# Performance work log

Hardware: AMD Instinct MI355X
Metric: run time of the kernel (lower is better)

The kernel has to match this reference:

```python
import jax, jax.numpy as jnp
import numpy as np

N = 20000          # num nodes
E = 320000         # num edges (avg degree 16)
IN = 128           # input feature dim
HID = 64           # layer1 out_channels per head
OUT = 128          # layer2 out_channels per head
H = 3              # attention heads
NEG = 0.15         # LeakyReLU negative slope
IN2 = IN + H * HID # layer2 input: concat(x, h1)


def setup_inputs() -> dict:
    key = jax.random.key(0)
    ks = jax.random.split(key, 12)
    lin = lambda k, fi, fo: (jax.random.normal(k, (fi, fo), jnp.float32) / np.float32(np.sqrt(fi)))
    return {
        "node_features": jax.random.normal(ks[0], (N, IN), jnp.float32),
        "Wl1": lin(ks[1], IN, H * HID),
        "bl1": jnp.zeros((H * HID,), jnp.float32),
        "Wr1": lin(ks[2], IN, H * HID),
        "br1": jnp.zeros((H * HID,), jnp.float32),
        "att1": jax.random.normal(ks[3], (H, HID), jnp.float32) / np.float32(np.sqrt(HID)),
        "bias1": jnp.zeros((H * HID,), jnp.float32),
        "Wl2": lin(ks[4], IN2, H * OUT),
        "bl2": jnp.zeros((H * OUT,), jnp.float32),
        "Wr2": lin(ks[5], IN2, H * OUT),
        "br2": jnp.zeros((H * OUT,), jnp.float32),
        "att2": jax.random.normal(ks[6], (H, OUT), jnp.float32) / np.float32(np.sqrt(OUT)),
        "bias2": jnp.zeros((OUT,), jnp.float32),
        "edge_index": jax.random.randint(ks[7], (2, E), 0, N, jnp.int64),
    }


def _gatv2(x, src, dst, Wl, bl, Wr, br, att, bias, concat):
    """PyG GATv2Conv (add_self_loops=False, eval/no dropout).
    src=edge_index[0] (message source j), dst=edge_index[1] (target i)."""
    n = x.shape[0]
    h, c = att.shape
    xl = (x @ Wl + bl).reshape(n, h, c)   # lin_l -> source/message features
    xr = (x @ Wr + br).reshape(n, h, c)   # lin_r -> target features
    e = xl[src] + xr[dst]                 # [E,H,C]
    e = jnp.where(e > 0, e, NEG * e)      # LeakyReLU
    logits = jnp.einsum('ehc,hc->eh', e, att)  # [E,H]
    # segment softmax over incoming edges of each dst node
    m = jax.ops.segment_max(logits, dst, num_segments=n)
    ex = jnp.exp(logits - m[dst])
    denom = jax.ops.segment_sum(ex, dst, num_segments=n)
    alpha = ex / (denom[dst] + 1e-16)
    out = jax.ops.segment_sum(xl[src] * alpha[:, :, None], dst, num_segments=n)  # [N,H,C]
    if concat:
        return out.reshape(n, h * c) + bias
    return out.mean(axis=1) + bias


def reference(node_features, Wl1, bl1, Wr1, br1, att1, bias1,
              Wl2, bl2, Wr2, br2, att2, bias2, edge_index):
    src, dst = edge_index[0], edge_index[1]
    h1 = jax.nn.relu(_gatv2(node_features, src, dst, Wl1, bl1, Wr1, br1, att1, bias1, True))
    h = jnp.concatenate([node_features, h1], axis=-1)  # [N, IN2]
    h2 = jax.nn.relu(_gatv2(h, src, dst, Wl2, bl2, Wr2, br2, att2, bias2, False))
    return h2
```

## Files before the change

kernel.cpp:

```cpp
#include <hip/hip_runtime.h>
#include <hip/hip_bf16.h>

#define NN 20000
#define EE 320000
#define IN 128
#define HID 64
#define OUTC 128
#define NH 3
#define NEG 0.15f
#define IN2 320
#define HO1 192
#define HO2 384
#define NB_SCAN 79
#define GRIDM128 157
#define LDA 72

typedef __hip_bfloat16 bf16;
typedef __attribute__((ext_vector_type(8))) short short8;
typedef __attribute__((ext_vector_type(4))) float f32x4;

__device__ __forceinline__ float bf2f(bf16 v) { return __bfloat162float(v); }
__device__ __forceinline__ bf16 f2bf(float v) { return __float2bfloat16(v); }
__device__ __forceinline__ float lrelu(float s) { return fmaxf(s, NEG * s); }
__device__ __forceinline__ float lo16(unsigned int d) {
    union { unsigned int u; float f; } c; c.u = d << 16; return c.f;
}
__device__ __forceinline__ float hi16(unsigned int d) {
    union { unsigned int u; float f; } c; c.u = d & 0xffff0000u; return c.f;
}

__global__ void k_count(const int* __restrict__ ei, int* __restrict__ cnt) {
    const int e = blockIdx.x * 256 + threadIdx.x;
    if (e < EE) atomicAdd(&cnt[ei[EE + e]], 1);
}

__global__ void k_scanA(const int* __restrict__ cnt, int* __restrict__ loc,
                        int* __restrict__ bsum) {
    __shared__ int sh[256];
    const int t = threadIdx.x;
    const int i = blockIdx.x * 256 + t;
    const int v = (i < NN) ? cnt[i] : 0;
    sh[t] = v; __syncthreads();
    for (int off = 1; off < 256; off <<= 1) {
        const int add = (t >= off) ? sh[t - off] : 0;
        __syncthreads();
        sh[t] += add; __syncthreads();
    }
    if (i < NN) loc[i] = sh[t];
    if (t == 255) bsum[blockIdx.x] = sh[255];
}

__global__ void k_scanB(int* __restrict__ bsum) {
    __shared__ int sh[128];
    const int t = threadIdx.x;
    const int v = (t < NB_SCAN) ? bsum[t] : 0;
    sh[t] = v; __syncthreads();
    for (int off = 1; off < 128; off <<= 1) {
        const int add = (t >= off) ? sh[t - off] : 0;
        __syncthreads();
        sh[t] += add; __syncthreads();
    }
    if (t < NB_SCAN) bsum[t] = sh[t] - v;
}

__global__ void k_scanC(const int* __restrict__ loc, const int* __restrict__ cnt,
                        const int* __restrict__ bsum, int* __restrict__ row_off,
                        int* __restrict__ fill) {
    const int i = blockIdx.x * 256 + threadIdx.x;
    if (i < NN) {
        const int ro = loc[i] - cnt[i] + bsum[blockIdx.x];
        row_off[i] = ro; fill[i] = ro;
    }
    if (i == 0) row_off[NN] = EE;
}

__global__ void k_scatter(const int* __restrict__ ei, int* __restrict__ fill,
                          int* __restrict__ csr_src) {
    const int e = blockIdx.x * 256 + threadIdx.x;
    if (e < EE) {
        const int p = atomicAdd(&fill[ei[EE + e]], 1);
        csr_src[p] = ei[e];
    }
}

__global__ void k_a2x(const float* __restrict__ x, bf16* __restrict__ xb) {
    const int idx = blockIdx.x * 256 + threadIdx.x;
    if (idx < NN * IN) xb[idx] = f2bf(x[idx]);
}

__global__ void k_wt(const float* __restrict__ Wl, const float* __restrict__ Wr,
                     int K, int NO, bf16* __restrict__ Wt) {
    const int idx = blockIdx.x * 256 + threadIdx.x;
    if (idx >= 2 * NO * K) return;
    const int n = idx / K, k = idx - n * K;
    const float* W = (n < NO) ? Wl : Wr;
    const int nn = (n < NO) ? n : n - NO;
    Wt[idx] = f2bf(W[(size_t)k * NO + nn]);
}

template <int K, int CH>
__launch_bounds__(256)
__global__ void gemm_mfma(const bf16* __restrict__ A0, int As0,
                          const bf16* __restrict__ A1, int As1,
                          const bf16* __restrict__ Wt,
                          const float* __restrict__ bl, const float* __restrict__ br,
                          int NO, size_t planeN,
                          bf16* __restrict__ outl, bf16* __restrict__ outr) {
    __shared__ bf16 Asm[128 * LDA];
    __shared__ bf16 Bsm[128 * LDA];
    const int tid = threadIdx.x;
    const int w = tid >> 6, lane = tid & 63;
    const int quad = lane >> 4, l15 = lane & 15;
    const int r0 = (w >> 1) * 64;
    const int c0 = (w & 1) * 64;
    const int m0 = blockIdx.x * 128;
    const int n0 = blockIdx.y * 128;

    f32x4 acc[4][4];
#pragma unroll
    for (int nt = 0; nt < 4; ++nt) {
        const int col = n0 + c0 + nt * 16 + l15;
        const float b = (col < NO) ? bl[col] : br[col - NO];
#pragma unroll
        for (int mt = 0; mt < 4; ++mt) acc[mt][nt] = (f32x4){b, b, b, b};
    }

    int arow[4]; size_t boff[4]; int soff[4];
#pragma unroll
    for (int q = 0; q < 4; ++q) {
        const int s = q * 256 + tid;
        int r = m0 + (s >> 3); if (r >= NN) r = NN - 1;
        arow[q] = r;
        boff[q] = (size_t)(n0 + (s >> 3)) * K + (s & 7) * 8;
        soff[q] = (s >> 3) * LDA + (s & 7) * 8;
    }

    short8 pa[4], pb[4];
#pragma unroll
    for (int q = 0; q < 4; ++q) {
        const int s = q * 256 + tid;
        pa[q] = *(const short8*)(A0 + (size_t)arow[q] * As0 + (s & 7) * 8);
        pb[q] = *(const short8*)(Wt + boff[q]);
    }

#pragma unroll
    for (int ks = 0; ks < K; ks += 64) {
#pragma unroll
        for (int q = 0; q < 4; ++q) {
            *(short8*)&Asm[soff[q]] = pa[q];
            *(short8*)&Bsm[soff[q]] = pb[q];
        }
        __syncthreads();
        if (ks + 64 < K) {
            const int nks = ks + 64;
#pragma unroll
            for (int q = 0; q < 4; ++q) {
                const int s = q * 256 + tid;
                const bf16* ap = (K <= 128 || nks < 128)
                    ? (A0 + (size_t)arow[q] * As0 + nks + (s & 7) * 8)
                    : (A1 + (size_t)arow[q] * As1 + (nks - 128) + (s & 7) * 8);
                pa[q] = *(const short8*)ap;
                pb[q] = *(const short8*)(Wt + boff[q] + nks);
            }
        }
#pragma unroll
        for (int kq = 0; kq < 2; ++kq) {
            short8 af[4], bf[4];
#pragma unroll
            for (int mt = 0; mt < 4; ++mt)
                af[mt] = *(const short8*)&Asm[(r0 + mt * 16 + l15) * LDA + kq * 32 + quad * 8];
#pragma unroll
            for (int nt = 0; nt < 4; ++nt)
                bf[nt] = *(const short8*)&Bsm[(c0 + nt * 16 + l15) * LDA + kq * 32 + quad * 8];
#pragma unroll
            for (int mt = 0; mt < 4; ++mt)
#pragma unroll
                for (int nt = 0; nt < 4; ++nt)
                    acc[mt][nt] = __builtin_amdgcn_mfma_f32_16x16x32_bf16(af[mt], bf[nt], acc[mt][nt], 0, 0, 0);
        }
        __syncthreads();
    }

#pragma unroll
    for (int mt = 0; mt < 4; ++mt)
#pragma unroll
    for (int nt = 0; nt < 4; ++nt) {
        const int col = n0 + c0 + nt * 16 + l15;
        const int cc = (col < NO) ? col : col - NO;
        bf16* o = (col < NO) ? outl : outr;
        const int h = cc / CH, c = cc - h * CH;
#pragma unroll
        for (int r = 0; r < 4; ++r) {
            const int row = m0 + r0 + mt * 16 + quad * 4 + r;
            if (row < NN) o[h * planeN + (size_t)row * CH + c] = f2bf(acc[mt][nt][r]);
        }
    }
}

__global__ void gather1(const int* __restrict__ row_off, const int* __restrict__ csr_src,
                        const bf16* __restrict__ xl, const bf16* __restrict__ xr,
                        const float* __restrict__ att, const float* __restrict__ bias,
                        bf16* __restrict__ h1) {
    const int i = blockIdx.x;
    const int w = threadIdx.x >> 6;
    const int lane = threadIdx.x & 63;
    const int g = lane >> 3;
    const int t = lane & 7;
    const unsigned short* xlu = (const unsigned short*)xl + (size_t)w * NN * HID;
    const unsigned short* xru = (const unsigned short*)xr + (size_t)w * NN * HID;
    float rv[8], av[8];
    {
        const uint4 ru = *(const uint4*)(xru + (size_t)i * HID + 8 * t);
        rv[0] = lo16(ru.x); rv[1] = hi16(ru.x);
        rv[2] = lo16(ru.y); rv[3] = hi16(ru.y);
        rv[4] = lo16(ru.z); rv[5] = hi16(ru.z);
        rv[6] = lo16(ru.w); rv[7] = hi16(ru.w);
#pragma unroll
        for (int c = 0; c < 8; ++c) av[c] = att[w * HID + 8 * t + c];
    }
    float acc[8] = {0.f, 0.f, 0.f, 0.f, 0.f, 0.f, 0.f, 0.f};
    float den = 0.f;
    const int kb = row_off[i], ke = row_off[i + 1];
    for (int p0 = kb; p0 < ke; p0 += 8) {
        const int idx = p0 + g;
        const int j = csr_src[idx < ke ? idx : ke - 1];
        const uint4 lu = *(const uint4*)(xlu + (size_t)j * HID + 8 * t);
        float lv[8];
        lv[0] = lo16(lu.x); lv[1] = hi16(lu.x);
        lv[2] = lo16(lu.y); lv[3] = hi16(lu.y);
        lv[4] = lo16(lu.z); lv[5] = hi16(lu.z);
        lv[6] = lo16(lu.w); lv[7] = hi16(lu.w);
        float p = 0.f;
#pragma unroll
        for (int c = 0; c < 8; ++c)
            p = fmaf(lrelu(lv[c] + rv[c]), av[c], p);
        p += __shfl_xor(p, 1, 64);
        p += __shfl_xor(p, 2, 64);
        p += __shfl_xor(p, 4, 64);
        const float ex = (idx < ke) ? __expf(p) : 0.f;
#pragma unroll
        for (int c = 0; c < 8; ++c) acc[c] = fmaf(ex, lv[c], acc[c]);
        den += ex;
    }
    __shared__ float part[NH][8][HID];
    __shared__ float dsh[NH][8];
    *(f32x4*)&part[w][g][8 * t]     = (f32x4){acc[0], acc[1], acc[2], acc[3]};
    *(f32x4*)&part[w][g][8 * t + 4] = (f32x4){acc[4], acc[5], acc[6], acc[7]};
    if (t == 0) dsh[w][g] = den;
    __syncthreads();
    const int o = threadIdx.x;
    const int hh = o >> 6, c = o & 63;
    float num = 0.f, dd = 0.f;
#pragma unroll
    for (int q = 0; q < 8; ++q) { num += part[hh][q][c]; dd += dsh[hh][q]; }
    const float v = num / (dd + 1e-16f) + bias[o];
    h1[(size_t)i * HO1 + o] = f2bf(v > 0.f ? v : 0.f);
}

__global__ void gather2(const int* __restrict__ row_off, const int* __restrict__ csr_src,
                        const bf16* __restrict__ xl2, const bf16* __restrict__ xr2,
                        const float* __restrict__ att2, const float* __restrict__ bias2,
                        float* __restrict__ out) {
    const int i = blockIdx.x;
    const int w = threadIdx.x >> 6;
    const int lane = threadIdx.x & 63;
    const int g = lane >> 4;
    const int t = lane & 15;
    const unsigned short* xlu = (const unsigned short*)xl2 + (size_t)w * NN * OUTC;
    const unsigned short* xru = (const unsigned short*)xr2 + (size_t)w * NN * OUTC;
    float rv[8], av[8];
    {
        const uint4 ru = *(const uint4*)(xru + (size_t)i * OUTC + 8 * t);
        rv[0] = lo16(ru.x); rv[1] = hi16(ru.x);
        rv[2] = lo16(ru.y); rv[3] = hi16(ru.y);
        rv[4] = lo16(ru.z); rv[5] = hi16(ru.z);
        rv[6] = lo16(ru.w); rv[7] = hi16(ru.w);
#pragma unroll
        for (int c = 0; c < 8; ++c) av[c] = att2[w * OUTC + 8 * t + c];
    }
    float acc[8] = {0.f, 0.f, 0.f, 0.f, 0.f, 0.f, 0.f, 0.f};
    float den = 0.f;
    const int kb = row_off[i], ke = row_off[i + 1];
    for (int p0 = kb; p0 < ke; p0 += 4) {
        const int idx = p0 + g;
        const int j = csr_src[idx < ke ? idx : ke - 1];
        const uint4 lu = *(const uint4*)(xlu + (size_t)j * OUTC + 8 * t);
        float lv[8];
        lv[0] = lo16(lu.x); lv[1] = hi16(lu.x);
        lv[2] = lo16(lu.y); lv[3] = hi16(lu.y);
        lv[4] = lo16(lu.z); lv[5] = hi16(lu.z);
        lv[6] = lo16(lu.w); lv[7] = hi16(lu.w);
        float p = 0.f;
#pragma unroll
        for (int c = 0; c < 8; ++c)
            p = fmaf(lrelu(lv[c] + rv[c]), av[c], p);
        p += __shfl_xor(p, 1, 64);
        p += __shfl_xor(p, 2, 64);
        p += __shfl_xor(p, 4, 64);
        p += __shfl_xor(p, 8, 64);
        const float ex = (idx < ke) ? __expf(p) : 0.f;
#pragma unroll
        for (int c = 0; c < 8; ++c) acc[c] = fmaf(ex, lv[c], acc[c]);
        den += ex;
    }
    __shared__ float part[NH][4][OUTC];
    __shared__ float dsh[NH][4];
    *(f32x4*)&part[w][g][8 * t]     = (f32x4){acc[0], acc[1], acc[2], acc[3]};
    *(f32x4*)&part[w][g][8 * t + 4] = (f32x4){acc[4], acc[5], acc[6], acc[7]};
    if (t == 0) dsh[w][g] = den;
    __syncthreads();
    if (threadIdx.x < OUTC) {
        const int c = threadIdx.x;
        float v = 0.f;
#pragma unroll
        for (int hh = 0; hh < NH; ++hh) {
            float num = part[hh][0][c] + part[hh][1][c] + part[hh][2][c] + part[hh][3][c];
            float dd  = dsh[hh][0] + dsh[hh][1] + dsh[hh][2] + dsh[hh][3];
            v += num / (dd + 1e-16f);
        }
        v = v * (1.f / 3.f) + bias2[c];
        out[(size_t)i * OUTC + c] = v > 0.f ? v : 0.f;
    }
}

extern "C" void kernel_launch(void* const* d_in, const int* in_sizes, int n_in,
                              void* d_out, int out_size, void* d_ws, size_t ws_size,
                              hipStream_t stream) {
    const float* x    = (const float*)d_in[0];
    const float* Wl1  = (const float*)d_in[1];
    const float* bl1  = (const float*)d_in[2];
    const float* Wr1  = (const float*)d_in[3];
    const float* br1  = (const float*)d_in[4];
    const float* att1 = (const float*)d_in[5];
    const float* bias1= (const float*)d_in[6];
    const float* Wl2  = (const float*)d_in[7];
    const float* bl2  = (const float*)d_in[8];
    const float* Wr2  = (const float*)d_in[9];
    const float* br2  = (const float*)d_in[10];
    const float* att2 = (const float*)d_in[11];
    const float* bias2= (const float*)d_in[12];
    const int*   ei   = (const int*)d_in[13];

    char* ws = (char*)d_ws;
    bf16*  xb     = (bf16*)(ws);
    bf16*  h1b    = (bf16*)(ws + 5120000);
    bf16*  xl1    = (bf16*)(ws + 12800000);
    bf16*  xr1    = (bf16*)(ws + 20480000);
    bf16*  xl2    = (bf16*)(ws + 12800000);
    bf16*  xr2    = (bf16*)(ws + 28160000);
    int*   cnt    = (int*)(ws + 43520000);
    int*   fill   = (int*)(ws + 43600000);
    int*   loc    = (int*)(ws + 43680000);
    int*   bsum   = (int*)(ws + 43760000);
    int*   rowoff = (int*)(ws + 43764096);
    int*   csrsrc = (int*)(ws + 43844104);
    bf16*  Wt1    = (bf16*)(ws + 45124112);
    bf16*  Wt2    = (bf16*)(ws + 45222416);

    k_a2x<<<(NN * IN + 255) / 256, 256, 0, stream>>>(x, xb);
    k_wt<<<(HO2 * IN + 255) / 256, 256, 0, stream>>>(Wl1, Wr1, IN, HO1, Wt1);
    k_wt<<<(2 * HO2 * IN2 + 255) / 256, 256, 0, stream>>>(Wl2, Wr2, IN2, HO2, Wt2);

    hipMemsetAsync(cnt, 0, NN * sizeof(int), stream);
    k_count<<<(EE + 255) / 256, 256, 0, stream>>>(ei, cnt);
    k_scanA<<<NB_SCAN, 256, 0, stream>>>(cnt, loc, bsum);
    k_scanB<<<1, 128, 0, stream>>>(bsum);
    k_scanC<<<NB_SCAN, 256, 0, stream>>>(loc, cnt, bsum, rowoff, fill);
    k_scatter<<<(EE + 255) / 256, 256, 0, stream>>>(ei, fill, csrsrc);

    gemm_mfma<IN, HID><<<dim3(GRIDM128, HO2 / 128), 256, 0, stream>>>(
        xb, IN, (const bf16*)nullptr, 0, Wt1, bl1, br1, HO1,
        (size_t)NN * HID, xl1, xr1);
    gather1<<<NN, 192, 0, stream>>>(rowoff, csrsrc, xl1, xr1, att1, bias1, h1b);

    gemm_mfma<IN2, OUTC><<<dim3(GRIDM128, 2 * HO2 / 128), 256, 0, stream>>>(
        xb, IN, h1b, HO1, Wt2, bl2, br2, HO2,
        (size_t)NN * OUTC, xl2, xr2);
    gather2<<<NN, 192, 0, stream>>>(rowoff, csrsrc, xl2, xr2, att2, bias2,
                                    (float*)d_out);
}
```

Baseline: 248.6 us.

## Pin attention heads to XCDs in gather kernels and fuse prep kernels

The gather kernels now launch one 64-thread block per (node, head) and map block IDs to heads so each head's feature plane is handled by a fixed subset of XCDs, keeping that head's data in the local L2. Gather2 writes per-head partial results (head 0 in fp32 to the output, heads 1-2 in bf16 scratch), and a new combine kernel averages them and applies bias and ReLU. The three prep kernels (x conversion and two weight transposes) are merged into one launch. In exchange there is an extra kernel pass over the output, bf16 rounding of the partials, and reliance on round-robin XCD block dispatch.

After: 261.4 us. +5.2%, slower.

```diff
diff --git a/kernel.cpp b/kernel.cpp
--- a/kernel.cpp
+++ b/kernel.cpp
@@ -83,19 +83,31 @@
     }
 }
 
-__global__ void k_a2x(const float* __restrict__ x, bf16* __restrict__ xb) {
-    const int idx = blockIdx.x * 256 + threadIdx.x;
-    if (idx < NN * IN) xb[idx] = f2bf(x[idx]);
-}
-
-__global__ void k_wt(const float* __restrict__ Wl, const float* __restrict__ Wr,
-                     int K, int NO, bf16* __restrict__ Wt) {
-    const int idx = blockIdx.x * 256 + threadIdx.x;
-    if (idx >= 2 * NO * K) return;
-    const int n = idx / K, k = idx - n * K;
-    const float* W = (n < NO) ? Wl : Wr;
-    const int nn = (n < NO) ? n : n - NO;
-    Wt[idx] = f2bf(W[(size_t)k * NO + nn]);
+#define PREP_XB (NN * IN)
+#define PREP_W1 (2 * HO1 * IN)
+#define PREP_W2 (2 * HO2 * IN2)
+__global__ void k_prep(const float* __restrict__ x,
+                       const float* __restrict__ Wl1, const float* __restrict__ Wr1,
+                       const float* __restrict__ Wl2, const float* __restrict__ Wr2,
+                       bf16* __restrict__ xb, bf16* __restrict__ Wt1,
+                       bf16* __restrict__ Wt2) {
+    int idx = blockIdx.x * 256 + threadIdx.x;
+    if (idx < PREP_XB) { xb[idx] = f2bf(x[idx]); return; }
+    idx -= PREP_XB;
+    if (idx < PREP_W1) {
+        const int n = idx / IN, k = idx - n * IN;
+        const float* W = (n < HO1) ? Wl1 : Wr1;
+        const int nn = (n < HO1) ? n : n - HO1;
+        Wt1[idx] = f2bf(W[(size_t)k * HO1 + nn]);
+        return;
+    }
+    idx -= PREP_W1;
+    if (idx < PREP_W2) {
+        const int n = idx / IN2, k = idx - n * IN2;
+        const float* W = (n < HO2) ? Wl2 : Wr2;
+        const int nn = (n < HO2) ? n : n - HO2;
+        Wt2[idx] = f2bf(W[(size_t)k * HO2 + nn]);
+    }
 }
 
 template <int K, int CH>
@@ -197,17 +209,27 @@
     }
 }
 
+__device__ __forceinline__ bool pin_map(int blk, int& h, int& i) {
+    const int xcd = blk & 7, slot = blk >> 3;
+    h = xcd % 3;
+    const int rank = xcd / 3;
+    const int cnt = (h == 2) ? 2 : 3;
+    i = slot * cnt + rank;
+    return i < NN;
+}
+#define PIN_GRID 80000
+
 __global__ void gather1(const int* __restrict__ row_off, const int* __restrict__ csr_src,
                         const bf16* __restrict__ xl, const bf16* __restrict__ xr,
                         const float* __restrict__ att, const float* __restrict__ bias,
                         bf16* __restrict__ h1) {
-    const int i = blockIdx.x;
-    const int w = threadIdx.x >> 6;
-    const int lane = threadIdx.x & 63;
+    int h, i;
+    if (!pin_map(blockIdx.x, h, i)) return;
+    const int lane = threadIdx.x;
     const int g = lane >> 3;
     const int t = lane & 7;
-    const unsigned short* xlu = (const unsigned short*)xl + (size_t)w * NN * HID;
-    const unsigned short* xru = (const unsigned short*)xr + (size_t)w * NN * HID;
+    const unsigned short* xlu = (const unsigned short*)xl + (size_t)h * NN * HID;
+    const unsigned short* xru = (const unsigned short*)xr + (size_t)h * NN * HID;
     float rv[8], av[8];
     {
         const uint4 ru = *(const uint4*)(xru + (size_t)i * HID + 8 * t);
@@ -216,7 +238,7 @@
         rv[4] = lo16(ru.z); rv[5] = hi16(ru.z);
         rv[6] = lo16(ru.w); rv[7] = hi16(ru.w);
 #pragma unroll
-        for (int c = 0; c < 8; ++c) av[c] = att[w * HID + 8 * t + c];
+        for (int c = 0; c < 8; ++c) av[c] = att[h * HID + 8 * t + c];
     }
     float acc[8] = {0.f, 0.f, 0.f, 0.f, 0.f, 0.f, 0.f, 0.f};
     float den = 0.f;
@@ -242,32 +264,32 @@
         for (int c = 0; c < 8; ++c) acc[c] = fmaf(ex, lv[c], acc[c]);
         den += ex;
     }
-    __shared__ float part[NH][8][HID];
-    __shared__ float dsh[NH][8];
-    *(f32x4*)&part[w][g][8 * t]     = (f32x4){acc[0], acc[1], acc[2], acc[3]};
-    *(f32x4*)&part[w][g][8 * t + 4] = (f32x4){acc[4], acc[5], acc[6], acc[7]};
-    if (t == 0) dsh[w][g] = den;
+    __shared__ float part[8][HID];
+    __shared__ float dsh[8];
+    *(f32x4*)&part[g][8 * t]     = (f32x4){acc[0], acc[1], acc[2], acc[3]};
+    *(f32x4*)&part[g][8 * t + 4] = (f32x4){acc[4], acc[5], acc[6], acc[7]};
+    if (t == 0) dsh[g] = den;
     __syncthreads();
-    const int o = threadIdx.x;
-    const int hh = o >> 6, c = o & 63;
+    const int c = lane;
     float num = 0.f, dd = 0.f;
 #pragma unroll
-    for (int q = 0; q < 8; ++q) { num += part[hh][q][c]; dd += dsh[hh][q]; }
-    const float v = num / (dd + 1e-16f) + bias[o];
-    h1[(size_t)i * HO1 + o] = f2bf(v > 0.f ? v : 0.f);
+    for (int q = 0; q < 8; ++q) { num += part[q][c]; dd += dsh[q]; }
+    const float v = num / (dd + 1e-16f) + bias[h * HID + c];
+    h1[(size_t)i * HO1 + h * HID + c] = f2bf(v > 0.f ? v : 0.f);
 }
 
 __global__ void gather2(const int* __restrict__ row_off, const int* __restrict__ csr_src,
                         const bf16* __restrict__ xl2, const bf16* __restrict__ xr2,
-                        const float* __restrict__ att2, const float* __restrict__ bias2,
-                        float* __restrict__ out) {
-    const int i = blockIdx.x;
-    const int w = threadIdx.x >> 6;
-    const int lane = threadIdx.x & 63;
+                        const float* __restrict__ att2,
+                        float* __restrict__ out0, bf16* __restrict__ p1b,
+                        bf16* __restrict__ p2b) {
+    int h, i;
+    if (!pin_map(blockIdx.x, h, i)) return;
+    const int lane = threadIdx.x;
     const int g = lane >> 4;
     const int t = lane & 15;
-    const unsigned short* xlu = (const unsigned short*)xl2 + (size_t)w * NN * OUTC;
-    const unsigned short* xru = (const unsigned short*)xr2 + (size_t)w * NN * OUTC;
+    const unsigned short* xlu = (const unsigned short*)xl2 + (size_t)h * NN * OUTC;
+    const unsigned short* xru = (const unsigned short*)xr2 + (size_t)h * NN * OUTC;
     float rv[8], av[8];
     {
         const uint4 ru = *(const uint4*)(xru + (size_t)i * OUTC + 8 * t);
@@ -276,7 +298,7 @@
         rv[4] = lo16(ru.z); rv[5] = hi16(ru.z);
         rv[6] = lo16(ru.w); rv[7] = hi16(ru.w);
 #pragma unroll
-        for (int c = 0; c < 8; ++c) av[c] = att2[w * OUTC + 8 * t + c];
+        for (int c = 0; c < 8; ++c) av[c] = att2[h * OUTC + 8 * t + c];
     }
     float acc[8] = {0.f, 0.f, 0.f, 0.f, 0.f, 0.f, 0.f, 0.f};
     float den = 0.f;
@@ -303,24 +325,31 @@
         for (int c = 0; c < 8; ++c) acc[c] = fmaf(ex, lv[c], acc[c]);
         den += ex;
     }
-    __shared__ float part[NH][4][OUTC];
-    __shared__ float dsh[NH][4];
-    *(f32x4*)&part[w][g][8 * t]     = (f32x4){acc[0], acc[1], acc[2], acc[3]};
-    *(f32x4*)&part[w][g][8 * t + 4] = (f32x4){acc[4], acc[5], acc[6], acc[7]};
-    if (t == 0) dsh[w][g] = den;
+    __shared__ float part[4][OUTC];
+    __shared__ float dsh[4];
+    *(f32x4*)&part[g][8 * t]     = (f32x4){acc[0], acc[1], acc[2], acc[3]};
+    *(f32x4*)&part[g][8 * t + 4] = (f32x4){acc[4], acc[5], acc[6], acc[7]};
+    if (t == 0) dsh[g] = den;
     __syncthreads();
-    if (threadIdx.x < OUTC) {
-        const int c = threadIdx.x;
-        float v = 0.f;
-#pragma unroll
-        for (int hh = 0; hh < NH; ++hh) {
-            float num = part[hh][0][c] + part[hh][1][c] + part[hh][2][c] + part[hh][3][c];
-            float dd  = dsh[hh][0] + dsh[hh][1] + dsh[hh][2] + dsh[hh][3];
-            v += num / (dd + 1e-16f);
-        }
-        v = v * (1.f / 3.f) + bias2[c];
-        out[(size_t)i * OUTC + c] = v > 0.f ? v : 0.f;
-    }
+    const float dd = dsh[0] + dsh[1] + dsh[2] + dsh[3];
+    const float inv = 1.f / (dd + 1e-16f);
+#pragma unroll
+    for (int u = 0; u < 2; ++u) {
+        const int c = lane + u * 64;
+        const float val = (part[0][c] + part[1][c] + part[2][c] + part[3][c]) * inv;
+        if (h == 0)      out0[(size_t)i * OUTC + c] = val;
+        else if (h == 1) p1b[(size_t)i * OUTC + c] = f2bf(val);
+        else             p2b[(size_t)i * OUTC + c] = f2bf(val);
+    }
+}
+
+__global__ void k_comb(float* __restrict__ out, const bf16* __restrict__ p1b,
+                       const bf16* __restrict__ p2b, const float* __restrict__ bias2) {
+    const int idx = blockIdx.x * 256 + threadIdx.x;
+    if (idx >= NN * OUTC) return;
+    const int c = idx & (OUTC - 1);
+    const float v = (out[idx] + bf2f(p1b[idx]) + bf2f(p2b[idx])) * (1.f / 3.f) + bias2[c];
+    out[idx] = v > 0.f ? v : 0.f;
 }
 
 extern "C" void kernel_launch(void* const* d_in, const int* in_sizes, int n_in,
@@ -348,6 +377,8 @@
     bf16*  xr1    = (bf16*)(ws + 20480000);
     bf16*  xl2    = (bf16*)(ws + 12800000);
     bf16*  xr2    = (bf16*)(ws + 28160000);
+    bf16*  p1b    = (bf16*)(ws);
+    bf16*  p2b    = (bf16*)(ws + 5120000);
     int*   cnt    = (int*)(ws + 43520000);
     int*   fill   = (int*)(ws + 43600000);
     int*   loc    = (int*)(ws + 43680000);
@@ -357,9 +388,8 @@
     bf16*  Wt1    = (bf16*)(ws + 45124112);
     bf16*  Wt2    = (bf16*)(ws + 45222416);
 
-    k_a2x<<<(NN * IN + 255) / 256, 256, 0, stream>>>(x, xb);
-    k_wt<<<(HO2 * IN + 255) / 256, 256, 0, stream>>>(Wl1, Wr1, IN, HO1, Wt1);
-    k_wt<<<(2 * HO2 * IN2 + 255) / 256, 256, 0, stream>>>(Wl2, Wr2, IN2, HO2, Wt2);
+    k_prep<<<(PREP_XB + PREP_W1 + PREP_W2 + 255) / 256, 256, 0, stream>>>(
+        x, Wl1, Wr1, Wl2, Wr2, xb, Wt1, Wt2);
 
     hipMemsetAsync(cnt, 0, NN * sizeof(int), stream);
     k_count<<<(EE + 255) / 256, 256, 0, stream>>>(ei, cnt);
@@ -371,11 +401,12 @@
     gemm_mfma<IN, HID><<<dim3(GRIDM128, HO2 / 128), 256, 0, stream>>>(
         xb, IN, (const bf16*)nullptr, 0, Wt1, bl1, br1, HO1,
         (size_t)NN * HID, xl1, xr1);
-    gather1<<<NN, 192, 0, stream>>>(rowoff, csrsrc, xl1, xr1, att1, bias1, h1b);
+    gather1<<<PIN_GRID, 64, 0, stream>>>(rowoff, csrsrc, xl1, xr1, att1, bias1, h1b);
 
     gemm_mfma<IN2, OUTC><<<dim3(GRIDM128, 2 * HO2 / 128), 256, 0, stream>>>(
         xb, IN, h1b, HO1, Wt2, bl2, br2, HO2,
         (size_t)NN * OUTC, xl2, xr2);
-    gather2<<<NN, 192, 0, stream>>>(rowoff, csrsrc, xl2, xr2, att2, bias2,
-                                    (float*)d_out);
-}
+    gather2<<<PIN_GRID, 64, 0, stream>>>(rowoff, csrsrc, xl2, xr2, att2,
+                                         (float*)d_out, p1b, p2b);
+    k_comb<<<(NN * OUTC + 255) / 256, 256, 0, stream>>>((float*)d_out, p1b, p2b, bias2);
+}
```
